# Optimization experiments

Measured on AMD Instinct MI355X. Metric: run time of the kernel, lower is better.

The kernel has to match this reference:

```python
import jax, jax.numpy as jnp
import numpy as np

INNER_LR = 0.01  # args['update_lr']
T, N, D, H = 100, 100, 1024, 8192


def setup_inputs() -> dict:
    key = jax.random.key(0)
    ks = jax.random.split(key, 6)
    return {
        "x_traj": jax.random.normal(ks[0], (T, D), jnp.float32),
        "y_traj": jax.random.normal(ks[1], (T, 1), jnp.float32),
        "x_rand": jax.random.normal(ks[2], (N, D), jnp.float32),
        "y_rand": jax.random.normal(ks[3], (N, 1), jnp.float32),
        # learned meta parameters of the columnar net
        "W": jax.random.normal(ks[4], (D, H), jnp.float32) * (1.0 / np.sqrt(D)),
        "b": jnp.zeros((H,), jnp.float32),
        # adaptation parameter (last-layer prediction weights)
        "w0": jax.random.normal(ks[5], (H,), jnp.float32) * 0.01,
    }


def reference(x_traj, y_traj, x_rand, y_rand, W, b, w0):
    lr = jnp.float32(INNER_LR)

    def net(x):
        h = jnp.tanh(x @ W + b)          # [H] hidden / rnn_state
        return h

    # ---- trajectory loop: update TH, online update of w, update TW ----
    def traj_step(carry, inp):
        w, TW_W, TW_b = carry
        x, tgt = inp
        h = net(x)
        y = jnp.dot(w, h)                # scalar prediction
        dact = 1.0 - h * h
        # update_TH: TH <- per-column grads of hidden wrt meta params
        TH_W = x[:, None] * dact[None, :]   # [D,H]
        TH_b = dact                          # [H]
        err = tgt - y
        # online_update (adaptation param), happens BEFORE update_TW
        w_new = w + lr * err * h
        # update_TW (uses post-update prediction params, old_state = h)
        TW_W = TW_W + lr * err * TH_W - lr * h[None, :] * (w_new[None, :] * TH_W + h[None, :] * TW_W)
        TW_b = TW_b + lr * err * TH_b - lr * h * (w_new * TH_b + h * TW_b)
        return (w_new, TW_W, TW_b), None

    init = (w0, jnp.zeros_like(W), jnp.zeros_like(b))
    (w_f, TW_W, TW_b), _ = jax.lax.scan(traj_step, init, (x_traj, y_traj[:, 0]))

    # ---- random (meta-loss) loop: accumulate meta-gradients ----
    def rand_step(carry, inp):
        gW, gb, loss = carry
        x, tgt = inp
        h = net(x)
        y = jnp.dot(w_f, h)
        dact = 1.0 - h * h
        TH_W = x[:, None] * dact[None, :]
        TH_b = dact
        err = tgt - y
        loss = loss + (y - tgt) ** 2     # F.mse_loss on scalars
        gW = gW + (-err) * (w_f[None, :] * TH_W + TW_W * h[None, :])
        gb = gb + (-err) * (w_f * TH_b + TW_b * h)
        return (gW, gb, loss), None

    init2 = (jnp.zeros_like(W), jnp.zeros_like(b), jnp.float32(0.0))
    (gW, gb, total_loss), _ = jax.lax.scan(rand_step, init2, (x_rand, y_rand[:, 0]))

    return (total_loss / N, gW, gb)
```

## Files before the change

kernel.cpp:

```cpp
#include <hip/hip_runtime.h>
#include <hip/hip_bf16.h>
#include <math.h>

#define TT 100
#define NN 100
#define DD 1024
#define HH 8192
#define ILR 0.01f

typedef short bf16x8 __attribute__((ext_vector_type(8)));
typedef float f32x4 __attribute__((ext_vector_type(4)));


__device__ __forceinline__ float wave_sum64(float v) {
#pragma unroll
  for (int off = 32; off; off >>= 1) v += __shfl_xor(v, off, 64);
  return v;
}

__device__ __forceinline__ unsigned short f2bf(float x) {
  __hip_bfloat16 b = __float2bfloat16(x);
  return *(unsigned short*)&b;
}
__device__ __forceinline__ float bf2f(unsigned short u) {
  __hip_bfloat16 b = *(__hip_bfloat16*)&u;
  return __bfloat162float(b);
}

__global__ __launch_bounds__(256) void k0_frag(const float* __restrict__ xt,
                                               const float* __restrict__ xr,
                                               unsigned short* __restrict__ XA2f,
                                               unsigned short* __restrict__ XT2f) {
  const int tx = threadIdx.x & 31;
  const int ty = threadIdx.x >> 5;
  const int m0 = blockIdx.x * 32;
  const int r0 = blockIdx.y * 32;
#pragma unroll
  for (int i = 0; i < 4; i++) {
    const int r = r0 + ty + i * 8;
    const int m = m0 + tx;
    float v = 0.f;
    if (r < 200) {
      const float* src = (r < TT) ? (xt + r * DD) : (xr + (r - TT) * DD);
      v = src[m];
    }
    const unsigned short h = f2bf(v);
    const unsigned short l = f2bf(v - bf2f(h));
    {
      const int idx = ((((r >> 4) * 32 + (m >> 5)) * 64) +
                       ((m >> 3) & 3) * 16 + (r & 15)) * 8 + (m & 7);
      XA2f[idx] = h;
      XA2f[idx + 262144] = l;
    }
    {
      const int idx = ((((m >> 4) * 8 + (r >> 5)) * 64) +
                       ((r >> 3) & 3) * 16 + (m & 15)) * 8 + (r & 7);
      XT2f[idx] = h;
      XT2f[idx + 262144] = l;
    }
  }
}

__global__ __launch_bounds__(256, 4) void k1_mfma5(const unsigned short* __restrict__ XA2f,
                                                   const float* __restrict__ W,
                                                   float* __restrict__ Cp) {
  __shared__ unsigned short Bsm[2 * 8192];
  const int tid = threadIdx.x;
  const int wid = tid >> 6;
  const int lane = tid & 63;
  const int flat = blockIdx.x;
  const int m8 = flat & 7;
  const int r_tile = (flat >> 3) & 3;
  const int z = (flat >> 5) & 1;
  const int chi = flat >> 6;
  const int c_tile = chi * 8 + m8;
  const int row0 = r_tile * 64;
  const int col0 = c_tile * 64;
  const int wr = wid >> 1;
  const int wc = wid & 1;

  const int cp = tid & 31;
  const int ko = tid >> 5;
  const int ct_s = cp >> 3;
  const int kb_s = ko >> 2;
  const int lane_s = (ko & 3) * 16 + ((2 * cp) & 15);
  const int sbase = ((ct_s * 2 + kb_s) * 64 + lane_s) * 8;

  f32x4 acc[2][2];
#pragma unroll
  for (int i = 0; i < 2; i++)
#pragma unroll
    for (int j = 0; j < 2; j++) {
      f32x4 zv = {0.f, 0.f, 0.f, 0.f};
      acc[i][j] = zv;
    }

  float2 wvA[8], wvB[8];
#define K1_LOADW(CH, REGS)                                                     \
  _Pragma("unroll") for (int e = 0; e < 8; e++) REGS[e] =                      \
      *(const float2*)&W[(size_t)(z * 512 + (CH) * 64 + ko * 8 + e) * HH +     \
                         col0 + cp * 2];
#define K1_CVT(REGS, BUF)                                                      \
  {                                                                            \
    bf16x8 H0, H1, L0, L1;                                                     \
    _Pragma("unroll") for (int e = 0; e < 8; e++) {                            \
      const float a = REGS[e].x, b = REGS[e].y;                                \
      const unsigned short ha = f2bf(a), hb = f2bf(b);                         \
      H0[e] = (short)ha;                                                       \
      L0[e] = (short)f2bf(a - bf2f(ha));                                       \
      H1[e] = (short)hb;                                                       \
      L1[e] = (short)f2bf(b - bf2f(hb));                                       \
    }                                                                          \
    unsigned short* d = Bsm + (BUF) * 8192 + sbase;                            \
    *(bf16x8*)d = H0;                                                          \
    *(bf16x8*)(d + 8) = H1;                                                    \
    *(bf16x8*)(d + 4096) = L0;                                                 \
    *(bf16x8*)(d + 4096 + 8) = L1;                                             \
  }
#define K1_MFMA(CHL, BUF)                                                      \
  _Pragma("unroll") for (int kb = 0; kb < 2; kb++) {                           \
    const int kbg = z * 16 + (CHL) * 2 + kb;                                   \
    bf16x8 ah[2], al[2], bh[2], bl[2];                                         \
    _Pragma("unroll") for (int mf = 0; mf < 2; mf++) {                         \
      const int tA = r_tile * 4 + wr * 2 + mf;                                 \
      const unsigned short* pa =                                               \
          XA2f + (size_t)((tA * 32 + kbg) * 64 + lane) * 8;                    \
      ah[mf] = *(const bf16x8*)pa;                                             \
      al[mf] = *(const bf16x8*)(pa + 262144);                                  \
    }                                                                          \
    _Pragma("unroll") for (int nf = 0; nf < 2; nf++) {                         \
      const int nfg = wc * 2 + nf;                                             \
      const unsigned short* pb =                                               \
          Bsm + (BUF) * 8192 + ((nfg * 2 + kb) * 64 + lane) * 8;               \
      bh[nf] = *(const bf16x8*)pb;                                             \
      bl[nf] = *(const bf16x8*)(pb + 4096);                                    \
    }                                                                          \
    _Pragma("unroll") for (int mf = 0; mf < 2; mf++)                           \
        _Pragma("unroll") for (int nf = 0; nf < 2; nf++) {                     \
      acc[mf][nf] = __builtin_amdgcn_mfma_f32_16x16x32_bf16(ah[mf], bh[nf],    \
                                                            acc[mf][nf], 0, 0, 0); \
      acc[mf][nf] = __builtin_amdgcn_mfma_f32_16x16x32_bf16(ah[mf], bl[nf],    \
                                                            acc[mf][nf], 0, 0, 0); \
      acc[mf][nf] = __builtin_amdgcn_mfma_f32_16x16x32_bf16(al[mf], bh[nf],    \
                                                            acc[mf][nf], 0, 0, 0); \
    }                                                                          \
  }

  K1_LOADW(0, wvA)
  K1_LOADW(1, wvB)
  K1_CVT(wvA, 0)
  __syncthreads();

#pragma unroll 1
  for (int ch2 = 0; ch2 < 8; ch2 += 2) {
    if (ch2 + 2 < 8) { K1_LOADW(ch2 + 2, wvA) }
    K1_MFMA(ch2, 0)
    K1_CVT(wvB, 1)
    __syncthreads();
    if (ch2 + 3 < 8) { K1_LOADW(ch2 + 3, wvB) }
    K1_MFMA(ch2 + 1, 1)
    if (ch2 + 2 < 8) {
      K1_CVT(wvA, 0)
      __syncthreads();
    }
  }
#undef K1_LOADW
#undef K1_CVT
#undef K1_MFMA

  const int l15 = lane & 15;
  const int drow = (lane >> 4) * 4;
#pragma unroll
  for (int mf = 0; mf < 2; mf++) {
    const int gr = row0 + wr * 32 + mf * 16 + drow;
#pragma unroll
    for (int nf = 0; nf < 2; nf++) {
      const int gc = col0 + wc * 32 + nf * 16 + l15;
#pragma unroll
      for (int r = 0; r < 4; r++) {
        const int row = gr + r;
        if (row < 200)
          Cp[(size_t)z * 2097152 + (size_t)row * HH + gc] = acc[mf][nf][r];
      }
    }
  }
}

__global__ __launch_bounds__(256) void k1b_comb(const float* __restrict__ Cp,
                                                const float* __restrict__ bias,
                                                float* __restrict__ Hall) {
  const int e4 = (blockIdx.x * 256 + threadIdx.x) * 4;
  const int row = e4 >> 13;
  const int col = e4 & (HH - 1);
  const float4 a = *(const float4*)(Cp + (size_t)row * HH + col);
  const float4 b = *(const float4*)(Cp + 2097152 + (size_t)row * HH + col);
  const float4 bb = *(const float4*)(bias + col);
  float4 h;
  h.x = tanhf(a.x + b.x + bb.x);
  h.y = tanhf(a.y + b.y + bb.y);
  h.z = tanhf(a.z + b.z + bb.z);
  h.w = tanhf(a.w + b.w + bb.w);
  *(float4*)(Hall + (size_t)row * HH + col) = h;
}

__global__ __launch_bounds__(64) void k2a_gram(const float* __restrict__ Ht,
                                               const float* __restrict__ w0,
                                               float* __restrict__ Gp,
                                               float* __restrict__ y0p) {
  __shared__ float red[64 * 65];
  const int task = blockIdx.x;
  const int z = blockIdx.y;
  const int lane = threadIdx.x;
  const int kb = z * 512;
  if (task < 91) {
    int a = 0, rem = task;
    while (rem >= 13 - a) { rem -= 13 - a; a++; }
    const int b = a + rem;
    const float* Ra = Ht + (size_t)(a * 8) * HH + kb;
    const float* Rb = Ht + (size_t)(b * 8) * HH + kb;
    float acc[8][8];
#pragma unroll
    for (int r = 0; r < 8; r++)
#pragma unroll
      for (int c = 0; c < 8; c++) acc[r][c] = 0.f;
#pragma unroll
    for (int i = 0; i < 2; i++) {
      const int k = (lane + i * 64) * 4;
      float4 x[8];
#pragma unroll
      for (int r = 0; r < 8; r++) x[r] = *(const float4*)(Ra + (size_t)r * HH + k);
#pragma unroll
      for (int c = 0; c < 8; c++) {
        const float4 u = *(const float4*)(Rb + (size_t)c * HH + k);
#pragma unroll
        for (int r = 0; r < 8; r++) {
          acc[r][c] = fmaf(x[r].x, u.x, acc[r][c]);
          acc[r][c] = fmaf(x[r].y, u.y, acc[r][c]);
          acc[r][c] = fmaf(x[r].z, u.z, acc[r][c]);
          acc[r][c] = fmaf(x[r].w, u.w, acc[r][c]);
        }
      }
    }
#pragma unroll
    for (int r = 0; r < 8; r++)
#pragma unroll
      for (int c = 0; c < 8; c++) red[lane * 65 + r * 8 + c] = acc[r][c];
    __syncthreads();
    float s = 0.f;
#pragma unroll
    for (int i = 0; i < 64; i++) s += red[i * 65 + lane];
    Gp[(size_t)task * 1024 + z * 64 + lane] = s;
  } else {
    const int a = task - 91;
    const float* R = Ht + (size_t)(a * 8) * HH + kb;
    float acc[8] = {0.f, 0.f, 0.f, 0.f, 0.f, 0.f, 0.f, 0.f};
#pragma unroll
    for (int i = 0; i < 2; i++) {
      const int k = (lane + i * 64) * 4;
      const float4 wvv = *(const float4*)(w0 + kb + k);
#pragma unroll
      for (int r = 0; r < 8; r++) {
        const float4 x = *(const float4*)(R + (size_t)r * HH + k);
        acc[r] += x.x * wvv.x + x.y * wvv.y + x.z * wvv.z + x.w * wvv.w;
      }
    }
#pragma unroll
    for (int r = 0; r < 8; r++) acc[r] = wave_sum64(acc[r]);
    if (lane == 0) {
#pragma unroll
      for (int r = 0; r < 8; r++) y0p[a * 128 + z * 8 + r] = acc[r];
    }
  }
}

__global__ __launch_bounds__(128) void k2b_reduce(const float* __restrict__ Gp,
                                                  const float* __restrict__ y0p,
                                                  float* __restrict__ G,
                                                  float* __restrict__ y0) {
  const int blk = blockIdx.x;
  const int t = threadIdx.x;
  if (blk < 91) {
    if (t < 64) {
      float s = 0.f;
#pragma unroll
      for (int z = 0; z < 16; z++) s += Gp[(size_t)blk * 1024 + z * 64 + t];
      int a = 0, rem = blk;
      while (rem >= 13 - a) { rem -= 13 - a; a++; }
      const int b = a + rem;
      const int gr = a * 8 + (t >> 3);
      const int gc = b * 8 + (t & 7);
      if (gr < 100 && gc < 100) {
        G[gr * 100 + gc] = s;
        G[gc * 100 + gr] = s;
      }
    }
  } else {
    if (t < 104) {
      float s = 0.f;
#pragma unroll
      for (int z = 0; z < 16; z++) s += y0p[(t >> 3) * 128 + z * 8 + (t & 7)];
      if (t < 100) y0[t] = s;
    }
  }
}

__global__ __launch_bounds__(256) void k3_solve2(const float* __restrict__ G,
                                                 const float* __restrict__ y0,
                                                 const float* __restrict__ ytraj,
                                                 float* __restrict__ errT) {
  __shared__ float Gs[100 * 100];
  __shared__ float rhs[100];
  const int tid = threadIdx.x;
  for (int idx = tid; idx < 10000; idx += 256) Gs[idx] = G[idx];
  if (tid < 100) rhs[tid] = ytraj[tid] - y0[tid];
  __syncthreads();
  if (tid >= 64) return;
  const int l = tid;
  float acc_lo = 0.f, acc_hi = 0.f;
  float err_lo = 0.f, err_hi = 0.f;
#pragma unroll 4
  for (int t = 0; t < TT; t++) {
    const float a = (t < 64) ? __shfl(acc_lo, t) : __shfl(acc_hi, t - 64);
    const float err = rhs[t] - ILR * a;
    if (t < 64) {
      if (l == t) err_lo = err;
    } else {
      if (l == t - 64) err_hi = err;
    }
    const float g_lo = Gs[t * 100 + l];
    if (l > t) acc_lo = fmaf(err, g_lo, acc_lo);
    if (l < 36) {
      const float g_hi = Gs[t * 100 + 64 + l];
      if (64 + l > t) acc_hi = fmaf(err, g_hi, acc_hi);
    }
  }
  errT[l] = err_lo;
  if (l < 36) errT[64 + l] = err_hi;
}

__global__ __launch_bounds__(64) void k4a_scan(const float* __restrict__ Ht,
                                               const float* __restrict__ errT,
                                               float* __restrict__ Sp,
                                               float* __restrict__ Pp) {
  __shared__ float es[20];
  const int c = blockIdx.y;
  const int t0 = c * 20;
  if (threadIdx.x < 20) es[threadIdx.x] = errT[t0 + threadIdx.x];
  __syncthreads();
  const int j = blockIdx.x * 64 + threadIdx.x;
  float h[20];
#pragma unroll
  for (int u = 0; u < 20; u++) h[u] = Ht[(size_t)(t0 + u) * HH + j];
  float S = 0.f, P = 1.f;
#pragma unroll
  for (int u = 0; u < 20; u++) S += es[u] * h[u];
#pragma unroll
  for (int u = 0; u < 20; u++) P *= (1.f - ILR * h[u] * h[u]);
  Sp[(size_t)c * HH + j] = S;
  Pp[(size_t)c * HH + j] = P;
}

__global__ __launch_bounds__(64) void k4b_emit(const float* __restrict__ Ht,
                                               const float* __restrict__ errT,
                                               const float* __restrict__ w0,
                                               const float* __restrict__ Sp,
                                               const float* __restrict__ Pp,
                                               float* __restrict__ Ct,
                                               float* __restrict__ wf) {
  __shared__ float es[20];
  const int c = blockIdx.y;
  const int t0 = c * 20;
  if (threadIdx.x < 20) es[threadIdx.x] = errT[t0 + threadIdx.x];
  __syncthreads();
  const int j = blockIdx.x * 64 + threadIdx.x;
  float Sv[5], Pv[5];
#pragma unroll
  for (int q = 0; q < 5; q++) {
    Sv[q] = Sp[(size_t)q * HH + j];
    Pv[q] = Pp[(size_t)q * HH + j];
  }
  float w = w0[j];
#pragma unroll
  for (int q = 0; q < 5; q++)
    if (q < c) w += ILR * Sv[q];
  float PA = 1.f;
#pragma unroll
  for (int q = 0; q < 5; q++)
    if (q > c) PA *= Pv[q];
  float h[20];
#pragma unroll
  for (int u = 0; u < 20; u++) h[u] = Ht[(size_t)(t0 + u) * HH + j];
  float ct[20];
#pragma unroll
  for (int u = 0; u < 20; u++) {
    const float e = es[u];
    w += ILR * e * h[u];
    ct[u] = ILR * (1.f - h[u] * h[u]) * (e - h[u] * w);
  }
  float r = PA;
#pragma unroll
  for (int u = 19; u >= 0; u--) {
    Ct[(size_t)(t0 + u) * HH + j] = ct[u] * r;
    r *= (1.f - ILR * h[u] * h[u]);
  }
  if (c == 4) wf[j] = w;
}

__global__ __launch_bounds__(256) void k5_pred(const float* __restrict__ Hr,
                                               const float* __restrict__ wf,
                                               const float* __restrict__ yr,
                                               float* __restrict__ e_r) {
  const int i = blockIdx.x;
  const int tid = threadIdx.x;
  const float* row = Hr + (size_t)i * HH;
  float p = 0.f;
#pragma unroll
  for (int c = tid * 4; c < HH; c += 1024) {
    const float4 h4 = *(const float4*)(row + c);
    const float4 w4 = *(const float4*)(wf + c);
    p += h4.x * w4.x + h4.y * w4.y + h4.z * w4.z + h4.w * w4.w;
  }
  p = wave_sum64(p);
  __shared__ float ps[4];
  if ((tid & 63) == 0) ps[tid >> 6] = p;
  __syncthreads();
  if (tid == 0) {
    const float y = ps[0] + ps[1] + ps[2] + ps[3];
    e_r[i] = y - yr[i];
  }
}

__global__ __launch_bounds__(64) void k6a_v(const float* __restrict__ Hr,
                                            const float* __restrict__ e_r,
                                            float* __restrict__ Vp) {
  __shared__ float es[20];
  const int c = blockIdx.y;
  const int i0 = c * 20;
  if (threadIdx.x < 20) es[threadIdx.x] = e_r[i0 + threadIdx.x];
  __syncthreads();
  const int j = blockIdx.x * 64 + threadIdx.x;
  float h[20];
#pragma unroll
  for (int u = 0; u < 20; u++) h[u] = Hr[(size_t)(i0 + u) * HH + j];
  float S = 0.f;
#pragma unroll
  for (int u = 0; u < 20; u++) S += es[u] * h[u];
  Vp[(size_t)c * HH + j] = S;
}

__global__ __launch_bounds__(256) void k6b_m(const float* __restrict__ Hr,
                                             const float* __restrict__ e_r,
                                             const float* __restrict__ wf,
                                             const float* __restrict__ Ct,
                                             const float* __restrict__ Vp,
                                             unsigned short* __restrict__ MT2f,
                                             float* __restrict__ gbp) {
  __shared__ float es[100];
  const int tid = threadIdx.x;
  for (int i = tid; i < 100; i += 256) es[i] = e_r[i];
  __syncthreads();
  const int j = blockIdx.x * 256 + tid;
  const int iMo = blockIdx.y;
  float v = 0.f;
#pragma unroll
  for (int c = 0; c < 5; c++) v += Vp[(size_t)c * HH + j];
  const float wfj = wf[j];
  float m[8];
#pragma unroll
  for (int e = 0; e < 8; e++) {
    const int iM = iMo * 8 + e;
    if (iM < 100) {
      m[e] = v * Ct[(size_t)iM * HH + j];
    } else if (iM < 200) {
      const float h = Hr[(size_t)(iM - 100) * HH + j];
      m[e] = es[iM - 100] * wfj * (1.f - h * h);
    } else {
      m[e] = 0.f;
    }
  }
  bf16x8 Hv, Lv;
  float gbs = 0.f;
#pragma unroll
  for (int e = 0; e < 8; e++) {
    const unsigned short hh = f2bf(m[e]);
    Hv[e] = (short)hh;
    Lv[e] = (short)f2bf(m[e] - bf2f(hh));
    gbs += m[e];
  }
  const int idx = (((j >> 4) * 8 + (iMo >> 2)) * 64 + (iMo & 3) * 16 + (j & 15)) * 8;
  *(bf16x8*)&MT2f[idx] = Hv;
  *(bf16x8*)&MT2f[idx + 2097152] = Lv;
  if (iMo < 25) gbp[(size_t)iMo * HH + j] = gbs;
}

__global__ __launch_bounds__(256) void k6c_gb(const float* __restrict__ gbp,
                                              const float* __restrict__ e_r,
                                              float* __restrict__ gb_out,
                                              float* __restrict__ loss_out) {
  const int tid = threadIdx.x;
  const int j = blockIdx.x * 256 + tid;
  float g = 0.f;
#pragma unroll
  for (int q = 0; q < 25; q++) g += gbp[(size_t)q * HH + j];
  gb_out[j] = g;
  if (blockIdx.x == 0 && tid < 64) {
    float s = e_r[tid] * e_r[tid];
    if (tid < 36) {
      const float q = e_r[tid + 64];
      s += q * q;
    }
    s = wave_sum64(s);
    if (tid == 0) loss_out[0] = s / (float)NN;
  }
}

__global__ __launch_bounds__(256) void k7_mfma2(const unsigned short* __restrict__ XT2f,
                                                const unsigned short* __restrict__ MT2f,
                                                float* __restrict__ gW) {
  const int tid = threadIdx.x;
  const int l = tid & 63;
  const int wid = tid >> 6;
  const int m0 = blockIdx.x * 128 + (wid >> 1) * 64;
  const int n0 = blockIdx.y * 128 + (wid & 1) * 64;
  const int tA0 = m0 >> 4;
  const int tN0 = n0 >> 4;

  f32x4 acc[4][4];
#pragma unroll
  for (int i = 0; i < 4; i++)
#pragma unroll
    for (int j = 0; j < 4; j++) {
      f32x4 z = {0.f, 0.f, 0.f, 0.f};
      acc[i][j] = z;
    }

#pragma unroll 2
  for (int kb = 0; kb < 8; kb++) {
    bf16x8 ah[4], al[4], bh[4], bl[4];
#pragma unroll
    for (int i = 0; i < 4; i++) {
      const unsigned short* pa = XT2f + (size_t)(((tA0 + i) * 8 + kb) * 64 + l) * 8;
      ah[i] = *(const bf16x8*)pa;
      al[i] = *(const bf16x8*)(pa + 262144);
      const unsigned short* pb = MT2f + (size_t)(((tN0 + i) * 8 + kb) * 64 + l) * 8;
      bh[i] = *(const bf16x8*)pb;
      bl[i] = *(const bf16x8*)(pb + 2097152);
    }
#pragma unroll
    for (int i = 0; i < 4; i++)
#pragma unroll
      for (int j = 0; j < 4; j++) {
        acc[i][j] = __builtin_amdgcn_mfma_f32_16x16x32_bf16(ah[i], bh[j], acc[i][j], 0, 0, 0);
        acc[i][j] = __builtin_amdgcn_mfma_f32_16x16x32_bf16(ah[i], bl[j], acc[i][j], 0, 0, 0);
        acc[i][j] = __builtin_amdgcn_mfma_f32_16x16x32_bf16(al[i], bh[j], acc[i][j], 0, 0, 0);
      }
  }
  const int l15 = l & 15;
  const int drow = (l >> 4) * 4;
#pragma unroll
  for (int i = 0; i < 4; i++)
#pragma unroll
    for (int j = 0; j < 4; j++) {
      float* dst = gW + (size_t)(m0 + i * 16 + drow) * HH + n0 + j * 16 + l15;
#pragma unroll
      for (int r = 0; r < 4; r++) dst[(size_t)r * HH] = acc[i][j][r];
    }
}

extern "C" void kernel_launch(void* const* d_in, const int* in_sizes, int n_in,
                              void* d_out, int out_size, void* d_ws, size_t ws_size,
                              hipStream_t stream) {
  (void)in_sizes; (void)n_in; (void)out_size; (void)ws_size;
  const float* xt = (const float*)d_in[0];
  const float* yt = (const float*)d_in[1];
  const float* xr = (const float*)d_in[2];
  const float* yr = (const float*)d_in[3];
  const float* W = (const float*)d_in[4];
  const float* bias = (const float*)d_in[5];
  const float* w0 = (const float*)d_in[6];
  float* out = (float*)d_out;
  float* ws = (float*)d_ws;

  float* Hall = ws;
  float* Ht = Hall;
  float* Hr = Hall + TT * HH;
  unsigned short* XA2f = (unsigned short*)(Hall + 200 * HH);
  unsigned short* XT2f = XA2f + 524288;
  float* scratch = (float*)(XT2f + 524288);
  float* Cp = scratch;
  float* Ct = scratch;
  unsigned short* MT2f = (unsigned short*)(scratch + 819200);
  float* Gp = scratch + 819200 + 2097152;
  float* y0p = Gp + 91 * 1024;
  float* Sp = y0p + 13 * 128;
  float* Pp = Sp + 5 * HH;
  float* Vp = Pp + 5 * HH;
  float* gbp = Vp + 5 * HH;
  float* G = scratch + 4194304;
  float* y0v = G + TT * TT;
  float* errT = y0v + TT;
  float* e_r = errT + TT;
  float* wf = e_r + NN;

  k0_frag<<<dim3(32, 8), 256, 0, stream>>>(xt, xr, XA2f, XT2f);
  k1_mfma5<<<1024, 256, 0, stream>>>(XA2f, W, Cp);
  k1b_comb<<<1600, 256, 0, stream>>>(Cp, bias, Hall);
  k2a_gram<<<dim3(104, 16), 64, 0, stream>>>(Ht, w0, Gp, y0p);
  k2b_reduce<<<92, 128, 0, stream>>>(Gp, y0p, G, y0v);
  k3_solve2<<<1, 256, 0, stream>>>(G, y0v, yt, errT);
  k4a_scan<<<dim3(128, 5), 64, 0, stream>>>(Ht, errT, Sp, Pp);
  k4b_emit<<<dim3(128, 5), 64, 0, stream>>>(Ht, errT, w0, Sp, Pp, Ct, wf);
  k5_pred<<<NN, 256, 0, stream>>>(Hr, wf, yr, e_r);
  k6a_v<<<dim3(128, 5), 64, 0, stream>>>(Hr, e_r, Vp);
  k6b_m<<<dim3(32, 32), 256, 0, stream>>>(Hr, e_r, wf, Ct, Vp, MT2f, gbp);
  k6c_gb<<<32, 256, 0, stream>>>(gbp, e_r, out + 1 + (size_t)DD * HH, out);
  k7_mfma2<<<dim3(8, 64), 256, 0, stream>>>(XT2f, MT2f, out + 1);
}
```

Before: 111.8 us.

## Compute random-set predictions via cross-Gram, fuse scans, merge gb into final GEMM

The random-set errors are now computed algebraically from a cross Gram matrix between random and trajectory hidden states plus w0 projections, inside the solve kernel. This removes the separate prediction kernel and its dependency on the final w. The two column-scan kernels are merged into one launch, and the gb reduction and loss are folded into other kernels, which cuts launch count. The first GEMM is also retiled to narrower 32-column tiles with higher occupancy, at the cost of extra Gram work and some change in floating-point order.

```diff
diff --git a/kernel.cpp b/kernel.cpp
--- a/kernel.cpp
+++ b/kernel.cpp
@@ -61,10 +61,10 @@
   }
 }
 
-__global__ __launch_bounds__(256, 4) void k1_mfma5(const unsigned short* __restrict__ XA2f,
+__global__ __launch_bounds__(256, 6) void k1_mfma6(const unsigned short* __restrict__ XA2f,
                                                    const float* __restrict__ W,
                                                    float* __restrict__ Cp) {
-  __shared__ unsigned short Bsm[2 * 8192];
+  __shared__ unsigned short Bsm[2 * 4096];
   const int tid = threadIdx.x;
   const int wid = tid >> 6;
   const int lane = tid & 63;
@@ -75,52 +75,41 @@
   const int chi = flat >> 6;
   const int c_tile = chi * 8 + m8;
   const int row0 = r_tile * 64;
-  const int col0 = c_tile * 64;
+  const int col0 = c_tile * 32;
   const int wr = wid >> 1;
   const int wc = wid & 1;
 
-  const int cp = tid & 31;
+  const int sc = tid & 31;
   const int ko = tid >> 5;
-  const int ct_s = cp >> 3;
-  const int kb_s = ko >> 2;
-  const int lane_s = (ko & 3) * 16 + ((2 * cp) & 15);
-  const int sbase = ((ct_s * 2 + kb_s) * 64 + lane_s) * 8;
-
-  f32x4 acc[2][2];
-#pragma unroll
-  for (int i = 0; i < 2; i++)
-#pragma unroll
-    for (int j = 0; j < 2; j++) {
-      f32x4 zv = {0.f, 0.f, 0.f, 0.f};
-      acc[i][j] = zv;
-    }
-
-  float2 wvA[8], wvB[8];
-#define K1_LOADW(CH, REGS)                                                     \
-  _Pragma("unroll") for (int e = 0; e < 8; e++) REGS[e] =                      \
-      *(const float2*)&W[(size_t)(z * 512 + (CH) * 64 + ko * 8 + e) * HH +     \
-                         col0 + cp * 2];
-#define K1_CVT(REGS, BUF)                                                      \
+  const int sbase = (((sc >> 4) * 2 + (ko >> 2)) * 64 + (ko & 3) * 16 + (sc & 15)) * 8;
+
+  f32x4 acc[2];
+#pragma unroll
+  for (int i = 0; i < 2; i++) {
+    f32x4 zv = {0.f, 0.f, 0.f, 0.f};
+    acc[i] = zv;
+  }
+
+  float wv[8];
+#define K1_LOADW(CH)                                                           \
+  _Pragma("unroll") for (int e = 0; e < 8; e++) wv[e] =                        \
+      W[(size_t)(z * 512 + (CH) * 64 + ko * 8 + e) * HH + col0 + sc];
+#define K1_CVT(BUF)                                                            \
   {                                                                            \
-    bf16x8 H0, H1, L0, L1;                                                     \
+    bf16x8 Hv, Lv;                                                             \
     _Pragma("unroll") for (int e = 0; e < 8; e++) {                            \
-      const float a = REGS[e].x, b = REGS[e].y;                                \
-      const unsigned short ha = f2bf(a), hb = f2bf(b);                         \
-      H0[e] = (short)ha;                                                       \
-      L0[e] = (short)f2bf(a - bf2f(ha));                                       \
-      H1[e] = (short)hb;                                                       \
-      L1[e] = (short)f2bf(b - bf2f(hb));                                       \
+      const unsigned short hh = f2bf(wv[e]);                                   \
+      Hv[e] = (short)hh;                                                       \
+      Lv[e] = (short)f2bf(wv[e] - bf2f(hh));                                   \
     }                                                                          \
-    unsigned short* d = Bsm + (BUF) * 8192 + sbase;                            \
-    *(bf16x8*)d = H0;                                                          \
-    *(bf16x8*)(d + 8) = H1;                                                    \
-    *(bf16x8*)(d + 4096) = L0;                                                 \
-    *(bf16x8*)(d + 4096 + 8) = L1;                                             \
+    unsigned short* d = Bsm + (BUF) * 4096 + sbase;                            \
+    *(bf16x8*)d = Hv;                                                          \
+    *(bf16x8*)(d + 2048) = Lv;                                                 \
   }
 #define K1_MFMA(CHL, BUF)                                                      \
   _Pragma("unroll") for (int kb = 0; kb < 2; kb++) {                           \
     const int kbg = z * 16 + (CHL) * 2 + kb;                                   \
-    bf16x8 ah[2], al[2], bh[2], bl[2];                                         \
+    bf16x8 ah[2], al[2], bh, bl;                                               \
     _Pragma("unroll") for (int mf = 0; mf < 2; mf++) {                         \
       const int tA = r_tile * 4 + wr * 2 + mf;                                 \
       const unsigned short* pa =                                               \
@@ -128,39 +117,29 @@
       ah[mf] = *(const bf16x8*)pa;                                             \
       al[mf] = *(const bf16x8*)(pa + 262144);                                  \
     }                                                                          \
-    _Pragma("unroll") for (int nf = 0; nf < 2; nf++) {                         \
-      const int nfg = wc * 2 + nf;                                             \
+    {                                                                          \
       const unsigned short* pb =                                               \
-          Bsm + (BUF) * 8192 + ((nfg * 2 + kb) * 64 + lane) * 8;               \
-      bh[nf] = *(const bf16x8*)pb;                                             \
-      bl[nf] = *(const bf16x8*)(pb + 4096);                                    \
+          Bsm + (BUF) * 4096 + ((wc * 2 + kb) * 64 + lane) * 8;                \
+      bh = *(const bf16x8*)pb;                                                 \
+      bl = *(const bf16x8*)(pb + 2048);                                        \
     }                                                                          \
-    _Pragma("unroll") for (int mf = 0; mf < 2; mf++)                           \
-        _Pragma("unroll") for (int nf = 0; nf < 2; nf++) {                     \
-      acc[mf][nf] = __builtin_amdgcn_mfma_f32_16x16x32_bf16(ah[mf], bh[nf],    \
-                                                            acc[mf][nf], 0, 0, 0); \
-      acc[mf][nf] = __builtin_amdgcn_mfma_f32_16x16x32_bf16(ah[mf], bl[nf],    \
-                                                            acc[mf][nf], 0, 0, 0); \
-      acc[mf][nf] = __builtin_amdgcn_mfma_f32_16x16x32_bf16(al[mf], bh[nf],    \
-                                                            acc[mf][nf], 0, 0, 0); \
+    _Pragma("unroll") for (int mf = 0; mf < 2; mf++) {                         \
+      acc[mf] = __builtin_amdgcn_mfma_f32_16x16x32_bf16(ah[mf], bh, acc[mf], 0, 0, 0); \
+      acc[mf] = __builtin_amdgcn_mfma_f32_16x16x32_bf16(ah[mf], bl, acc[mf], 0, 0, 0); \
+      acc[mf] = __builtin_amdgcn_mfma_f32_16x16x32_bf16(al[mf], bh, acc[mf], 0, 0, 0); \
     }                                                                          \
   }
 
-  K1_LOADW(0, wvA)
-  K1_LOADW(1, wvB)
-  K1_CVT(wvA, 0)
+  K1_LOADW(0)
+  K1_CVT(0)
   __syncthreads();
 
 #pragma unroll 1
-  for (int ch2 = 0; ch2 < 8; ch2 += 2) {
-    if (ch2 + 2 < 8) { K1_LOADW(ch2 + 2, wvA) }
-    K1_MFMA(ch2, 0)
-    K1_CVT(wvB, 1)
-    __syncthreads();
-    if (ch2 + 3 < 8) { K1_LOADW(ch2 + 3, wvB) }
-    K1_MFMA(ch2 + 1, 1)
-    if (ch2 + 2 < 8) {
-      K1_CVT(wvA, 0)
+  for (int ch = 0; ch < 8; ch++) {
+    if (ch < 7) { K1_LOADW(ch + 1) }
+    K1_MFMA(ch, ch & 1)
+    if (ch < 7) {
+      K1_CVT((ch + 1) & 1)
       __syncthreads();
     }
   }
@@ -173,15 +152,12 @@
 #pragma unroll
   for (int mf = 0; mf < 2; mf++) {
     const int gr = row0 + wr * 32 + mf * 16 + drow;
-#pragma unroll
-    for (int nf = 0; nf < 2; nf++) {
-      const int gc = col0 + wc * 32 + nf * 16 + l15;
-#pragma unroll
-      for (int r = 0; r < 4; r++) {
-        const int row = gr + r;
-        if (row < 200)
-          Cp[(size_t)z * 2097152 + (size_t)row * HH + gc] = acc[mf][nf][r];
-      }
+    const int gc = col0 + wc * 16 + l15;
+#pragma unroll
+    for (int r = 0; r < 4; r++) {
+      const int row = gr + r;
+      if (row < 200)
+        Cp[(size_t)z * 2097152 + (size_t)row * HH + gc] = acc[mf][r];
     }
   }
 }
@@ -203,21 +179,40 @@
   *(float4*)(Hall + (size_t)row * HH + col) = h;
 }
 
-__global__ __launch_bounds__(64) void k2a_gram(const float* __restrict__ Ht,
-                                               const float* __restrict__ w0,
-                                               float* __restrict__ Gp,
-                                               float* __restrict__ y0p) {
+__global__ __launch_bounds__(64) void k2a_gram2(const float* __restrict__ Hall,
+                                                const float* __restrict__ w0,
+                                                float* __restrict__ Gp,
+                                                float* __restrict__ CGp,
+                                                float* __restrict__ y0p,
+                                                float* __restrict__ qp) {
   __shared__ float red[64 * 65];
   const int task = blockIdx.x;
-  const int z = blockIdx.y;
+  const int zz = blockIdx.y;
   const int lane = threadIdx.x;
-  const int kb = z * 512;
-  if (task < 91) {
-    int a = 0, rem = task;
-    while (rem >= 13 - a) { rem -= 13 - a; a++; }
-    const int b = a + rem;
-    const float* Ra = Ht + (size_t)(a * 8) * HH + kb;
-    const float* Rb = Ht + (size_t)(b * 8) * HH + kb;
+  const int kb = zz * 512;
+  const float* Ht = Hall;
+  const float* Hr = Hall + (size_t)TT * HH;
+
+  const bool is_pair = (task < 91);
+  const bool is_cross = (task >= 104 && task < 273);
+  if (is_pair || is_cross) {
+    const float *Ra, *Rb;
+    float* outp;
+    if (is_pair) {
+      int a = 0, rem = task;
+      while (rem >= 13 - a) { rem -= 13 - a; a++; }
+      const int b = a + rem;
+      Ra = Ht + (size_t)(a * 8) * HH + kb;
+      Rb = Ht + (size_t)(b * 8) * HH + kb;
+      outp = Gp + (size_t)task * 1024;
+    } else {
+      const int tc = task - 104;
+      const int ar = tc / 13;
+      const int bt = tc % 13;
+      Ra = Hr + (size_t)(ar * 8) * HH + kb;
+      Rb = Ht + (size_t)(bt * 8) * HH + kb;
+      outp = CGp + (size_t)tc * 1024;
+    }
     float acc[8][8];
 #pragma unroll
     for (int r = 0; r < 8; r++)
@@ -249,10 +244,12 @@
     float s = 0.f;
 #pragma unroll
     for (int i = 0; i < 64; i++) s += red[i * 65 + lane];
-    Gp[(size_t)task * 1024 + z * 64 + lane] = s;
+    outp[zz * 64 + lane] = s;
   } else {
-    const int a = task - 91;
-    const float* R = Ht + (size_t)(a * 8) * HH + kb;
+    const bool is_y0 = (task < 104);
+    const int a = is_y0 ? (task - 91) : (task - 273);
+    const float* R = (is_y0 ? Ht : Hr) + (size_t)(a * 8) * HH + kb;
+    float* outp = (is_y0 ? y0p : qp) + a * 128 + zz * 8;
     float acc[8] = {0.f, 0.f, 0.f, 0.f, 0.f, 0.f, 0.f, 0.f};
 #pragma unroll
     for (int i = 0; i < 2; i++) {
@@ -268,22 +265,26 @@
     for (int r = 0; r < 8; r++) acc[r] = wave_sum64(acc[r]);
     if (lane == 0) {
 #pragma unroll
-      for (int r = 0; r < 8; r++) y0p[a * 128 + z * 8 + r] = acc[r];
-    }
-  }
-}
-
-__global__ __launch_bounds__(128) void k2b_reduce(const float* __restrict__ Gp,
-                                                  const float* __restrict__ y0p,
-                                                  float* __restrict__ G,
-                                                  float* __restrict__ y0) {
+      for (int r = 0; r < 8; r++) outp[r] = acc[r];
+    }
+  }
+}
+
+__global__ __launch_bounds__(128) void k2b_reduce2(const float* __restrict__ Gp,
+                                                   const float* __restrict__ CGp,
+                                                   const float* __restrict__ y0p,
+                                                   const float* __restrict__ qp,
+                                                   float* __restrict__ G,
+                                                   float* __restrict__ CGT,
+                                                   float* __restrict__ y0,
+                                                   float* __restrict__ qv) {
   const int blk = blockIdx.x;
   const int t = threadIdx.x;
   if (blk < 91) {
     if (t < 64) {
       float s = 0.f;
 #pragma unroll
-      for (int z = 0; z < 16; z++) s += Gp[(size_t)blk * 1024 + z * 64 + t];
+      for (int zz = 0; zz < 16; zz++) s += Gp[(size_t)blk * 1024 + zz * 64 + t];
       int a = 0, rem = blk;
       while (rem >= 13 - a) { rem -= 13 - a; a++; }
       const int b = a + rem;
@@ -294,70 +295,132 @@
         G[gc * 100 + gr] = s;
       }
     }
+  } else if (blk < 260) {
+    if (t < 64) {
+      const int tc = blk - 91;
+      float s = 0.f;
+#pragma unroll
+      for (int zz = 0; zz < 16; zz++) s += CGp[(size_t)tc * 1024 + zz * 64 + t];
+      const int i = (tc / 13) * 8 + (t >> 3);
+      const int tt = (tc % 13) * 8 + (t & 7);
+      if (i < 100 && tt < 100) CGT[tt * 104 + i] = s;
+    }
+  } else if (blk == 260) {
+    if (t < 104) {
+      float s = 0.f;
+#pragma unroll
+      for (int zz = 0; zz < 16; zz++) s += y0p[(t >> 3) * 128 + zz * 8 + (t & 7)];
+      if (t < 100) y0[t] = s;
+    }
   } else {
     if (t < 104) {
       float s = 0.f;
 #pragma unroll
-      for (int z = 0; z < 16; z++) s += y0p[(t >> 3) * 128 + z * 8 + (t & 7)];
-      if (t < 100) y0[t] = s;
-    }
-  }
-}
-
-__global__ __launch_bounds__(256) void k3_solve2(const float* __restrict__ G,
+      for (int zz = 0; zz < 16; zz++) s += qp[(t >> 3) * 128 + zz * 8 + (t & 7)];
+      if (t < 100) qv[t] = s;
+    }
+  }
+}
+
+__global__ __launch_bounds__(256) void k3_solve3(const float* __restrict__ G,
                                                  const float* __restrict__ y0,
                                                  const float* __restrict__ ytraj,
-                                                 float* __restrict__ errT) {
+                                                 const float* __restrict__ yr,
+                                                 const float* __restrict__ qv,
+                                                 const float* __restrict__ CGT,
+                                                 float* __restrict__ errT,
+                                                 float* __restrict__ e_r,
+                                                 float* __restrict__ loss_out) {
   __shared__ float Gs[100 * 100];
   __shared__ float rhs[100];
+  __shared__ float esL[100];
+  __shared__ float e2[100];
   const int tid = threadIdx.x;
   for (int idx = tid; idx < 10000; idx += 256) Gs[idx] = G[idx];
   if (tid < 100) rhs[tid] = ytraj[tid] - y0[tid];
   __syncthreads();
-  if (tid >= 64) return;
-  const int l = tid;
-  float acc_lo = 0.f, acc_hi = 0.f;
-  float err_lo = 0.f, err_hi = 0.f;
+  if (tid < 64) {
+    const int l = tid;
+    float acc_lo = 0.f, acc_hi = 0.f;
+    float err_lo = 0.f, err_hi = 0.f;
 #pragma unroll 4
-  for (int t = 0; t < TT; t++) {
-    const float a = (t < 64) ? __shfl(acc_lo, t) : __shfl(acc_hi, t - 64);
-    const float err = rhs[t] - ILR * a;
-    if (t < 64) {
-      if (l == t) err_lo = err;
-    } else {
-      if (l == t - 64) err_hi = err;
-    }
-    const float g_lo = Gs[t * 100 + l];
-    if (l > t) acc_lo = fmaf(err, g_lo, acc_lo);
+    for (int t = 0; t < TT; t++) {
+      const float a = (t < 64) ? __shfl(acc_lo, t) : __shfl(acc_hi, t - 64);
+      const float err = rhs[t] - ILR * a;
+      if (t < 64) {
+        if (l == t) err_lo = err;
+      } else {
+        if (l == t - 64) err_hi = err;
+      }
+      const float g_lo = Gs[t * 100 + l];
+      if (l > t) acc_lo = fmaf(err, g_lo, acc_lo);
+      if (l < 36) {
+        const float g_hi = Gs[t * 100 + 64 + l];
+        if (64 + l > t) acc_hi = fmaf(err, g_hi, acc_hi);
+      }
+    }
+    errT[l] = err_lo;
+    esL[l] = err_lo;
     if (l < 36) {
-      const float g_hi = Gs[t * 100 + 64 + l];
-      if (64 + l > t) acc_hi = fmaf(err, g_hi, acc_hi);
-    }
-  }
-  errT[l] = err_lo;
-  if (l < 36) errT[64 + l] = err_hi;
-}
-
-__global__ __launch_bounds__(64) void k4a_scan(const float* __restrict__ Ht,
+      errT[64 + l] = err_hi;
+      esL[64 + l] = err_hi;
+    }
+  }
+  __syncthreads();
+  if (tid < 100) {
+    float er = qv[tid];
+#pragma unroll 1
+    for (int t0 = 0; t0 < 100; t0 += 10) {
+      float cg[10];
+#pragma unroll
+      for (int u = 0; u < 10; u++) cg[u] = CGT[(t0 + u) * 104 + tid];
+#pragma unroll
+      for (int u = 0; u < 10; u++) er = fmaf(ILR * esL[t0 + u], cg[u], er);
+    }
+    er -= yr[tid];
+    e_r[tid] = er;
+    e2[tid] = er * er;
+  }
+  __syncthreads();
+  if (tid < 64) {
+    float s = e2[tid];
+    if (tid < 36) s += e2[tid + 64];
+    s = wave_sum64(s);
+    if (tid == 0) loss_out[0] = s / (float)NN;
+  }
+}
+
+__global__ __launch_bounds__(64) void k46_scan(const float* __restrict__ Hall,
                                                const float* __restrict__ errT,
+                                               const float* __restrict__ e_r,
                                                float* __restrict__ Sp,
-                                               float* __restrict__ Pp) {
+                                               float* __restrict__ Pp,
+                                               float* __restrict__ Vp) {
   __shared__ float es[20];
-  const int c = blockIdx.y;
+  const int y = blockIdx.y;
+  const bool isV = (y >= 5);
+  const int c = isV ? (y - 5) : y;
   const int t0 = c * 20;
-  if (threadIdx.x < 20) es[threadIdx.x] = errT[t0 + threadIdx.x];
+  if (threadIdx.x < 20)
+    es[threadIdx.x] = isV ? e_r[t0 + threadIdx.x] : errT[t0 + threadIdx.x];
   __syncthreads();
   const int j = blockIdx.x * 64 + threadIdx.x;
+  const float* base = Hall + (isV ? (size_t)TT * HH : 0);
   float h[20];
 #pragma unroll
-  for (int u = 0; u < 20; u++) h[u] = Ht[(size_t)(t0 + u) * HH + j];
-  float S = 0.f, P = 1.f;
+  for (int u = 0; u < 20; u++) h[u] = base[(size_t)(t0 + u) * HH + j];
+  float S = 0.f;
 #pragma unroll
   for (int u = 0; u < 20; u++) S += es[u] * h[u];
-#pragma unroll
-  for (int u = 0; u < 20; u++) P *= (1.f - ILR * h[u] * h[u]);
-  Sp[(size_t)c * HH + j] = S;
-  Pp[(size_t)c * HH + j] = P;
+  if (isV) {
+    Vp[(size_t)c * HH + j] = S;
+  } else {
+    float P = 1.f;
+#pragma unroll
+    for (int u = 0; u < 20; u++) P *= (1.f - ILR * h[u] * h[u]);
+    Sp[(size_t)c * HH + j] = S;
+    Pp[(size_t)c * HH + j] = P;
+  }
 }
 
 __global__ __launch_bounds__(64) void k4b_emit(const float* __restrict__ Ht,
@@ -406,48 +469,6 @@
   if (c == 4) wf[j] = w;
 }
 
-__global__ __launch_bounds__(256) void k5_pred(const float* __restrict__ Hr,
-                                               const float* __restrict__ wf,
-                                               const float* __restrict__ yr,
-                                               float* __restrict__ e_r) {
-  const int i = blockIdx.x;
-  const int tid = threadIdx.x;
-  const float* row = Hr + (size_t)i * HH;
-  float p = 0.f;
-#pragma unroll
-  for (int c = tid * 4; c < HH; c += 1024) {
-    const float4 h4 = *(const float4*)(row + c);
-    const float4 w4 = *(const float4*)(wf + c);
-    p += h4.x * w4.x + h4.y * w4.y + h4.z * w4.z + h4.w * w4.w;
-  }
-  p = wave_sum64(p);
-  __shared__ float ps[4];
-  if ((tid & 63) == 0) ps[tid >> 6] = p;
-  __syncthreads();
-  if (tid == 0) {
-    const float y = ps[0] + ps[1] + ps[2] + ps[3];
-    e_r[i] = y - yr[i];
-  }
-}
-
-__global__ __launch_bounds__(64) void k6a_v(const float* __restrict__ Hr,
-                                            const float* __restrict__ e_r,
-                                            float* __restrict__ Vp) {
-  __shared__ float es[20];
-  const int c = blockIdx.y;
-  const int i0 = c * 20;
-  if (threadIdx.x < 20) es[threadIdx.x] = e_r[i0 + threadIdx.x];
-  __syncthreads();
-  const int j = blockIdx.x * 64 + threadIdx.x;
-  float h[20];
-#pragma unroll
-  for (int u = 0; u < 20; u++) h[u] = Hr[(size_t)(i0 + u) * HH + j];
-  float S = 0.f;
-#pragma unroll
-  for (int u = 0; u < 20; u++) S += es[u] * h[u];
-  Vp[(size_t)c * HH + j] = S;
-}
-
 __global__ __launch_bounds__(256) void k6b_m(const float* __restrict__ Hr,
                                              const float* __restrict__ e_r,
                                              const float* __restrict__ wf,
@@ -493,31 +514,19 @@
   if (iMo < 25) gbp[(size_t)iMo * HH + j] = gbs;
 }
 
-__global__ __launch_bounds__(256) void k6c_gb(const float* __restrict__ gbp,
-                                              const float* __restrict__ e_r,
-                                              float* __restrict__ gb_out,
-                                              float* __restrict__ loss_out) {
+__global__ __launch_bounds__(256) void k7_mfma3(const unsigned short* __restrict__ XT2f,
+                                                const unsigned short* __restrict__ MT2f,
+                                                const float* __restrict__ gbp,
+                                                float* __restrict__ gW,
+                                                float* __restrict__ gb_out) {
   const int tid = threadIdx.x;
-  const int j = blockIdx.x * 256 + tid;
-  float g = 0.f;
-#pragma unroll
-  for (int q = 0; q < 25; q++) g += gbp[(size_t)q * HH + j];
-  gb_out[j] = g;
-  if (blockIdx.x == 0 && tid < 64) {
-    float s = e_r[tid] * e_r[tid];
-    if (tid < 36) {
-      const float q = e_r[tid + 64];
-      s += q * q;
-    }
-    s = wave_sum64(s);
-    if (tid == 0) loss_out[0] = s / (float)NN;
-  }
-}
-
-__global__ __launch_bounds__(256) void k7_mfma2(const unsigned short* __restrict__ XT2f,
-                                                const unsigned short* __restrict__ MT2f,
-                                                float* __restrict__ gW) {
-  const int tid = threadIdx.x;
+  if (blockIdx.x == 0 && tid < 128) {
+    const int j = blockIdx.y * 128 + tid;
+    float g = 0.f;
+#pragma unroll
+    for (int q = 0; q < 25; q++) g += gbp[(size_t)q * HH + j];
+    gb_out[j] = g;
+  }
   const int l = tid & 63;
   const int wid = tid >> 6;
   const int m0 = blockIdx.x * 128 + (wid >> 1) * 64;
@@ -596,23 +605,25 @@
   float* Pp = Sp + 5 * HH;
   float* Vp = Pp + 5 * HH;
   float* gbp = Vp + 5 * HH;
+  float* CGp = gbp + 25 * HH;
+  float* qp = CGp + 169 * 1024;
   float* G = scratch + 4194304;
   float* y0v = G + TT * TT;
   float* errT = y0v + TT;
   float* e_r = errT + TT;
   float* wf = e_r + NN;
+  float* CGT = wf + HH;
+  float* qv = CGT + 10816;
 
   k0_frag<<<dim3(32, 8), 256, 0, stream>>>(xt, xr, XA2f, XT2f);
-  k1_mfma5<<<1024, 256, 0, stream>>>(XA2f, W, Cp);
+  k1_mfma6<<<2048, 256, 0, stream>>>(XA2f, W, Cp);
   k1b_comb<<<1600, 256, 0, stream>>>(Cp, bias, Hall);
-  k2a_gram<<<dim3(104, 16), 64, 0, stream>>>(Ht, w0, Gp, y0p);
-  k2b_reduce<<<92, 128, 0, stream>>>(Gp, y0p, G, y0v);
-  k3_solve2<<<1, 256, 0, stream>>>(G, y0v, yt, errT);
-  k4a_scan<<<dim3(128, 5), 64, 0, stream>>>(Ht, errT, Sp, Pp);
+  k2a_gram2<<<dim3(286, 16), 64, 0, stream>>>(Hall, w0, Gp, CGp, y0p, qp);
+  k2b_reduce2<<<262, 128, 0, stream>>>(Gp, CGp, y0p, qp, G, CGT, y0v, qv);
+  k3_solve3<<<1, 256, 0, stream>>>(G, y0v, yt, yr, qv, CGT, errT, e_r, out);
+  k46_scan<<<dim3(128, 10), 64, 0, stream>>>(Hall, errT, e_r, Sp, Pp, Vp);
   k4b_emit<<<dim3(128, 5), 64, 0, stream>>>(Ht, errT, w0, Sp, Pp, Ct, wf);
-  k5_pred<<<NN, 256, 0, stream>>>(Hr, wf, yr, e_r);
-  k6a_v<<<dim3(128, 5), 64, 0, stream>>>(Hr, e_r, Vp);
   k6b_m<<<dim3(32, 32), 256, 0, stream>>>(Hr, e_r, wf, Ct, Vp, MT2f, gbp);
-  k6c_gb<<<32, 256, 0, stream>>>(gbp, e_r, out + 1 + (size_t)DD * HH, out);
-  k7_mfma2<<<dim3(8, 64), 256, 0, stream>>>(XT2f, MT2f, out + 1);
-}
+  k7_mfma3<<<dim3(8, 64), 256, 0, stream>>>(XT2f, MT2f, gbp, out + 1,
+                                            out + 1 + (size_t)DD * HH);
+}
```

Measured after the change: 112.6 us. No clear change (+0.7%).

## Drop split-K in hidden GEMM, fuse bias+tanh epilogue, fold small kernels

Applied to the files above, without the earlier changes.

The hidden-state GEMM no longer splits K into two partial products written to scratch. Each block now covers the full K with 32-column tiles and applies bias plus tanh directly in its epilogue, which removes the separate combine kernel and its scratch traffic. The gb reduction moves into the gW MFMA kernel and the loss reduction into k6a, so two fewer kernels are launched. The cost is a longer serial K loop per block with a thinner N tile, and the small reductions now add work to the blocks that host them.

```diff
diff --git a/kernel.cpp b/kernel.cpp
--- a/kernel.cpp
+++ b/kernel.cpp
@@ -61,66 +61,55 @@
   }
 }
 
-__global__ __launch_bounds__(256, 4) void k1_mfma5(const unsigned short* __restrict__ XA2f,
+__global__ __launch_bounds__(256, 4) void k1_mfma7(const unsigned short* __restrict__ XA2f,
                                                    const float* __restrict__ W,
-                                                   float* __restrict__ Cp) {
-  __shared__ unsigned short Bsm[2 * 8192];
+                                                   const float* __restrict__ bias,
+                                                   float* __restrict__ Hall) {
+  __shared__ unsigned short Bsm[2 * 4096];
   const int tid = threadIdx.x;
   const int wid = tid >> 6;
   const int lane = tid & 63;
   const int flat = blockIdx.x;
   const int m8 = flat & 7;
   const int r_tile = (flat >> 3) & 3;
-  const int z = (flat >> 5) & 1;
-  const int chi = flat >> 6;
+  const int chi = flat >> 5;
   const int c_tile = chi * 8 + m8;
   const int row0 = r_tile * 64;
-  const int col0 = c_tile * 64;
+  const int col0 = c_tile * 32;
   const int wr = wid >> 1;
   const int wc = wid & 1;
 
-  const int cp = tid & 31;
+  const int sc = tid & 31;
   const int ko = tid >> 5;
-  const int ct_s = cp >> 3;
-  const int kb_s = ko >> 2;
-  const int lane_s = (ko & 3) * 16 + ((2 * cp) & 15);
-  const int sbase = ((ct_s * 2 + kb_s) * 64 + lane_s) * 8;
-
-  f32x4 acc[2][2];
-#pragma unroll
-  for (int i = 0; i < 2; i++)
-#pragma unroll
-    for (int j = 0; j < 2; j++) {
-      f32x4 zv = {0.f, 0.f, 0.f, 0.f};
-      acc[i][j] = zv;
-    }
-
-  float2 wvA[8], wvB[8];
-#define K1_LOADW(CH, REGS)                                                     \
-  _Pragma("unroll") for (int e = 0; e < 8; e++) REGS[e] =                      \
-      *(const float2*)&W[(size_t)(z * 512 + (CH) * 64 + ko * 8 + e) * HH +     \
-                         col0 + cp * 2];
-#define K1_CVT(REGS, BUF)                                                      \
+  const int sbase = (((sc >> 4) * 2 + (ko >> 2)) * 64 + (ko & 3) * 16 + (sc & 15)) * 8;
+
+  f32x4 acc[2];
+#pragma unroll
+  for (int i = 0; i < 2; i++) {
+    f32x4 zv = {0.f, 0.f, 0.f, 0.f};
+    acc[i] = zv;
+  }
+
+  float wv[8];
+#define K1_LOADW(CH)                                                           \
+  _Pragma("unroll") for (int e = 0; e < 8; e++) wv[e] =                        \
+      W[(size_t)((CH) * 64 + ko * 8 + e) * HH + col0 + sc];
+#define K1_CVT(BUF)                                                            \
   {                                                                            \
-    bf16x8 H0, H1, L0, L1;                                                     \
+    bf16x8 Hv, Lv;                                                             \
     _Pragma("unroll") for (int e = 0; e < 8; e++) {                            \
-      const float a = REGS[e].x, b = REGS[e].y;                                \
-      const unsigned short ha = f2bf(a), hb = f2bf(b);                         \
-      H0[e] = (short)ha;                                                       \
-      L0[e] = (short)f2bf(a - bf2f(ha));                                       \
-      H1[e] = (short)hb;                                                       \
-      L1[e] = (short)f2bf(b - bf2f(hb));                                       \
+      const unsigned short hh = f2bf(wv[e]);                                   \
+      Hv[e] = (short)hh;                                                       \
+      Lv[e] = (short)f2bf(wv[e] - bf2f(hh));                                   \
     }                                                                          \
-    unsigned short* d = Bsm + (BUF) * 8192 + sbase;                            \
-    *(bf16x8*)d = H0;                                                          \
-    *(bf16x8*)(d + 8) = H1;                                                    \
-    *(bf16x8*)(d + 4096) = L0;                                                 \
-    *(bf16x8*)(d + 4096 + 8) = L1;                                             \
+    unsigned short* d = Bsm + (BUF) * 4096 + sbase;                            \
+    *(bf16x8*)d = Hv;                                                          \
+    *(bf16x8*)(d + 2048) = Lv;                                                 \
   }
 #define K1_MFMA(CHL, BUF)                                                      \
   _Pragma("unroll") for (int kb = 0; kb < 2; kb++) {                           \
-    const int kbg = z * 16 + (CHL) * 2 + kb;                                   \
-    bf16x8 ah[2], al[2], bh[2], bl[2];                                         \
+    const int kbg = (CHL) * 2 + kb;                                            \
+    bf16x8 ah[2], al[2], bh, bl;                                               \
     _Pragma("unroll") for (int mf = 0; mf < 2; mf++) {                         \
       const int tA = r_tile * 4 + wr * 2 + mf;                                 \
       const unsigned short* pa =                                               \
@@ -128,39 +117,29 @@
       ah[mf] = *(const bf16x8*)pa;                                             \
       al[mf] = *(const bf16x8*)(pa + 262144);                                  \
     }                                                                          \
-    _Pragma("unroll") for (int nf = 0; nf < 2; nf++) {                         \
-      const int nfg = wc * 2 + nf;                                             \
+    {                                                                          \
       const unsigned short* pb =                                               \
-          Bsm + (BUF) * 8192 + ((nfg * 2 + kb) * 64 + lane) * 8;               \
-      bh[nf] = *(const bf16x8*)pb;                                             \
-      bl[nf] = *(const bf16x8*)(pb + 4096);                                    \
+          Bsm + (BUF) * 4096 + ((wc * 2 + kb) * 64 + lane) * 8;                \
+      bh = *(const bf16x8*)pb;                                                 \
+      bl = *(const bf16x8*)(pb + 2048);                                        \
     }                                                                          \
-    _Pragma("unroll") for (int mf = 0; mf < 2; mf++)                           \
-        _Pragma("unroll") for (int nf = 0; nf < 2; nf++) {                     \
-      acc[mf][nf] = __builtin_amdgcn_mfma_f32_16x16x32_bf16(ah[mf], bh[nf],    \
-                                                            acc[mf][nf], 0, 0, 0); \
-      acc[mf][nf] = __builtin_amdgcn_mfma_f32_16x16x32_bf16(ah[mf], bl[nf],    \
-                                                            acc[mf][nf], 0, 0, 0); \
-      acc[mf][nf] = __builtin_amdgcn_mfma_f32_16x16x32_bf16(al[mf], bh[nf],    \
-                                                            acc[mf][nf], 0, 0, 0); \
+    _Pragma("unroll") for (int mf = 0; mf < 2; mf++) {                         \
+      acc[mf] = __builtin_amdgcn_mfma_f32_16x16x32_bf16(ah[mf], bh, acc[mf], 0, 0, 0); \
+      acc[mf] = __builtin_amdgcn_mfma_f32_16x16x32_bf16(ah[mf], bl, acc[mf], 0, 0, 0); \
+      acc[mf] = __builtin_amdgcn_mfma_f32_16x16x32_bf16(al[mf], bh, acc[mf], 0, 0, 0); \
     }                                                                          \
   }
 
-  K1_LOADW(0, wvA)
-  K1_LOADW(1, wvB)
-  K1_CVT(wvA, 0)
+  K1_LOADW(0)
+  K1_CVT(0)
   __syncthreads();
 
 #pragma unroll 1
-  for (int ch2 = 0; ch2 < 8; ch2 += 2) {
-    if (ch2 + 2 < 8) { K1_LOADW(ch2 + 2, wvA) }
-    K1_MFMA(ch2, 0)
-    K1_CVT(wvB, 1)
-    __syncthreads();
-    if (ch2 + 3 < 8) { K1_LOADW(ch2 + 3, wvB) }
-    K1_MFMA(ch2 + 1, 1)
-    if (ch2 + 2 < 8) {
-      K1_CVT(wvA, 0)
+  for (int ch = 0; ch < 16; ch++) {
+    if (ch < 15) { K1_LOADW(ch + 1) }
+    K1_MFMA(ch, ch & 1)
+    if (ch < 15) {
+      K1_CVT((ch + 1) & 1)
       __syncthreads();
     }
   }
@@ -173,34 +152,15 @@
 #pragma unroll
   for (int mf = 0; mf < 2; mf++) {
     const int gr = row0 + wr * 32 + mf * 16 + drow;
-#pragma unroll
-    for (int nf = 0; nf < 2; nf++) {
-      const int gc = col0 + wc * 32 + nf * 16 + l15;
-#pragma unroll
-      for (int r = 0; r < 4; r++) {
-        const int row = gr + r;
-        if (row < 200)
-          Cp[(size_t)z * 2097152 + (size_t)row * HH + gc] = acc[mf][nf][r];
-      }
-    }
-  }
-}
-
-__global__ __launch_bounds__(256) void k1b_comb(const float* __restrict__ Cp,
-                                                const float* __restrict__ bias,
-                                                float* __restrict__ Hall) {
-  const int e4 = (blockIdx.x * 256 + threadIdx.x) * 4;
-  const int row = e4 >> 13;
-  const int col = e4 & (HH - 1);
-  const float4 a = *(const float4*)(Cp + (size_t)row * HH + col);
-  const float4 b = *(const float4*)(Cp + 2097152 + (size_t)row * HH + col);
-  const float4 bb = *(const float4*)(bias + col);
-  float4 h;
-  h.x = tanhf(a.x + b.x + bb.x);
-  h.y = tanhf(a.y + b.y + bb.y);
-  h.z = tanhf(a.z + b.z + bb.z);
-  h.w = tanhf(a.w + b.w + bb.w);
-  *(float4*)(Hall + (size_t)row * HH + col) = h;
+    const int gc = col0 + wc * 16 + l15;
+    const float bv = bias[gc];
+#pragma unroll
+    for (int r = 0; r < 4; r++) {
+      const int row = gr + r;
+      if (row < 200)
+        Hall[(size_t)row * HH + gc] = tanhf(acc[mf][r] + bv);
+    }
+  }
 }
 
 __global__ __launch_bounds__(64) void k2a_gram(const float* __restrict__ Ht,
@@ -432,12 +392,23 @@
 
 __global__ __launch_bounds__(64) void k6a_v(const float* __restrict__ Hr,
                                             const float* __restrict__ e_r,
-                                            float* __restrict__ Vp) {
+                                            float* __restrict__ Vp,
+                                            float* __restrict__ loss_out) {
   __shared__ float es[20];
   const int c = blockIdx.y;
   const int i0 = c * 20;
   if (threadIdx.x < 20) es[threadIdx.x] = e_r[i0 + threadIdx.x];
   __syncthreads();
+  if (blockIdx.x == 0 && c == 0) {
+    const int l = threadIdx.x;
+    float s = e_r[l] * e_r[l];
+    if (l < 36) {
+      const float q = e_r[l + 64];
+      s += q * q;
+    }
+    s = wave_sum64(s);
+    if (l == 0) loss_out[0] = s / (float)NN;
+  }
   const int j = blockIdx.x * 64 + threadIdx.x;
   float h[20];
 #pragma unroll
@@ -493,31 +464,19 @@
   if (iMo < 25) gbp[(size_t)iMo * HH + j] = gbs;
 }
 
-__global__ __launch_bounds__(256) void k6c_gb(const float* __restrict__ gbp,
-                                              const float* __restrict__ e_r,
-                                              float* __restrict__ gb_out,
-                                              float* __restrict__ loss_out) {
+__global__ __launch_bounds__(256) void k7_mfma3(const unsigned short* __restrict__ XT2f,
+                                                const unsigned short* __restrict__ MT2f,
+                                                const float* __restrict__ gbp,
+                                                float* __restrict__ gW,
+                                                float* __restrict__ gb_out) {
   const int tid = threadIdx.x;
-  const int j = blockIdx.x * 256 + tid;
-  float g = 0.f;
-#pragma unroll
-  for (int q = 0; q < 25; q++) g += gbp[(size_t)q * HH + j];
-  gb_out[j] = g;
-  if (blockIdx.x == 0 && tid < 64) {
-    float s = e_r[tid] * e_r[tid];
-    if (tid < 36) {
-      const float q = e_r[tid + 64];
-      s += q * q;
-    }
-    s = wave_sum64(s);
-    if (tid == 0) loss_out[0] = s / (float)NN;
-  }
-}
-
-__global__ __launch_bounds__(256) void k7_mfma2(const unsigned short* __restrict__ XT2f,
-                                                const unsigned short* __restrict__ MT2f,
-                                                float* __restrict__ gW) {
-  const int tid = threadIdx.x;
+  if (blockIdx.x == 0 && tid < 128) {
+    const int j = blockIdx.y * 128 + tid;
+    float g = 0.f;
+#pragma unroll
+    for (int q = 0; q < 25; q++) g += gbp[(size_t)q * HH + j];
+    gb_out[j] = g;
+  }
   const int l = tid & 63;
   const int wid = tid >> 6;
   const int m0 = blockIdx.x * 128 + (wid >> 1) * 64;
@@ -587,7 +546,6 @@
   unsigned short* XA2f = (unsigned short*)(Hall + 200 * HH);
   unsigned short* XT2f = XA2f + 524288;
   float* scratch = (float*)(XT2f + 524288);
-  float* Cp = scratch;
   float* Ct = scratch;
   unsigned short* MT2f = (unsigned short*)(scratch + 819200);
   float* Gp = scratch + 819200 + 2097152;
@@ -596,23 +554,22 @@
   float* Pp = Sp + 5 * HH;
   float* Vp = Pp + 5 * HH;
   float* gbp = Vp + 5 * HH;
-  float* G = scratch + 4194304;
+  float* G = gbp + 25 * HH;
   float* y0v = G + TT * TT;
   float* errT = y0v + TT;
   float* e_r = errT + TT;
   float* wf = e_r + NN;
 
   k0_frag<<<dim3(32, 8), 256, 0, stream>>>(xt, xr, XA2f, XT2f);
-  k1_mfma5<<<1024, 256, 0, stream>>>(XA2f, W, Cp);
-  k1b_comb<<<1600, 256, 0, stream>>>(Cp, bias, Hall);
+  k1_mfma7<<<1024, 256, 0, stream>>>(XA2f, W, bias, Hall);
   k2a_gram<<<dim3(104, 16), 64, 0, stream>>>(Ht, w0, Gp, y0p);
   k2b_reduce<<<92, 128, 0, stream>>>(Gp, y0p, G, y0v);
   k3_solve2<<<1, 256, 0, stream>>>(G, y0v, yt, errT);
   k4a_scan<<<dim3(128, 5), 64, 0, stream>>>(Ht, errT, Sp, Pp);
   k4b_emit<<<dim3(128, 5), 64, 0, stream>>>(Ht, errT, w0, Sp, Pp, Ct, wf);
   k5_pred<<<NN, 256, 0, stream>>>(Hr, wf, yr, e_r);
-  k6a_v<<<dim3(128, 5), 64, 0, stream>>>(Hr, e_r, Vp);
+  k6a_v<<<dim3(128, 5), 64, 0, stream>>>(Hr, e_r, Vp, out);
   k6b_m<<<dim3(32, 32), 256, 0, stream>>>(Hr, e_r, wf, Ct, Vp, MT2f, gbp);
-  k6c_gb<<<32, 256, 0, stream>>>(gbp, e_r, out + 1 + (size_t)DD * HH, out);
-  k7_mfma2<<<dim3(8, 64), 256, 0, stream>>>(XT2f, MT2f, out + 1);
-}
+  k7_mfma3<<<dim3(8, 64), 256, 0, stream>>>(XT2f, MT2f, gbp, out + 1,
+                                            out + 1 + (size_t)DD * HH);
+}
```

Result: faster. 105.7 us, median of 2 (-5.4%).
